# Kernel optimization log

Measured on AMD Instinct MI355X. Metric: run time of the kernel, lower is better.

## Reference

```python
import jax, jax.numpy as jnp
import numpy as np

N = 100000
NUM_CLASSES = 10
EPS = 1e-16
NEG_SLOPE = 0.2


def gat_conv(x, src, dst, W, a_src, a_dst, bias, heads, out_ch, concat):
    # x: [N, F_in]; src/dst: [E] (message flows src -> dst, PyG convention)
    n = x.shape[0]
    h = (x @ W).reshape(n, heads, out_ch)              # [N, H, C]
    al = jnp.sum(h * a_src, axis=-1)                   # [N, H] source attention term
    ar = jnp.sum(h * a_dst, axis=-1)                   # [N, H] target attention term
    e = jax.nn.leaky_relu(al[src] + ar[dst], NEG_SLOPE)  # [E, H]
    # segment softmax over incoming edges of each dst node
    m = jax.ops.segment_max(e, dst, num_segments=n)    # [N, H]
    ex = jnp.exp(e - m[dst])                           # [E, H]
    denom = jax.ops.segment_sum(ex, dst, num_segments=n)  # [N, H]
    alpha = ex / (denom[dst] + EPS)                    # [E, H]
    msg = h[src] * alpha[..., None]                    # [E, H, C]
    out = jax.ops.segment_sum(msg, dst, num_segments=n)   # [N, H, C]
    out = out.reshape(n, heads * out_ch) if concat else out.mean(axis=1)
    return out + bias


def setup_inputs() -> dict:
    key = jax.random.key(0)
    ks = jax.random.split(key, 10)
    F_in, H1, C1 = 512, 8, 8
    x = jax.random.normal(ks[0], (N, F_in), dtype=jnp.float32)
    edge_index = jax.random.randint(ks[1], (2, 1600000), 0, N, dtype=jnp.int64)
    s = 0.05
    return {
        "x": x,
        "edge_index": edge_index,
        "W1": jax.random.normal(ks[2], (F_in, H1 * C1), dtype=jnp.float32) * s,
        "a_src1": jax.random.normal(ks[3], (H1, C1), dtype=jnp.float32) * s,
        "a_dst1": jax.random.normal(ks[4], (H1, C1), dtype=jnp.float32) * s,
        "b1": jnp.zeros((H1 * C1,), dtype=jnp.float32),
        "W2": jax.random.normal(ks[5], (H1 * C1, NUM_CLASSES), dtype=jnp.float32) * s,
        "a_src2": jax.random.normal(ks[6], (1, NUM_CLASSES), dtype=jnp.float32) * s,
        "a_dst2": jax.random.normal(ks[7], (1, NUM_CLASSES), dtype=jnp.float32) * s,
        "b2": jnp.zeros((NUM_CLASSES,), dtype=jnp.float32),
    }


def reference(x, edge_index, W1, a_src1, a_dst1, b1, W2, a_src2, a_dst2, b2):
    # add self-loops (GATConv default add_self_loops=True)
    loops = jnp.arange(N, dtype=edge_index.dtype)
    src = jnp.concatenate([edge_index[0], loops])
    dst = jnp.concatenate([edge_index[1], loops])
    # eval mode: dropout(p=0.6) is identity
    h = gat_conv(x, src, dst, W1, a_src1, a_dst1, b1, heads=8, out_ch=8, concat=True)
    h = jax.nn.elu(h)
    out = gat_conv(h, src, dst, W2, a_src2, a_dst2, b2, heads=1, out_ch=NUM_CLASSES, concat=True)
    return jax.nn.log_softmax(out, axis=1)
```

## Files before the change

### kernel.cpp

```cpp
#include <hip/hip_runtime.h>
#include <math.h>

#define NN 100000
#define NEDGE 1600000
#define NTOT 1700000
#define FIN 512
#define NH1 8
#define NC1 8
#define F1 64
#define NC2 10
#define SLOPE 0.2f
#define EPSF 1e-16f
#define SCAN_BLK 1024
#define NB ((NN + SCAN_BLK - 1) / SCAN_BLK)

typedef short short8 __attribute__((ext_vector_type(8)));
typedef float f32x4 __attribute__((ext_vector_type(4)));

__device__ __forceinline__ float lrelu(float x) { return x > 0.f ? x : SLOPE * x; }
__device__ __forceinline__ float eluf(float x) { return x > 0.f ? x : __expf(x) - 1.f; }

__device__ __forceinline__ unsigned short f2bf_rne(float f) {
    unsigned int u = __float_as_uint(f);
    unsigned int r = (u + 0x7FFFu + ((u >> 16) & 1u)) >> 16;
    return (unsigned short)r;
}
__device__ __forceinline__ float bf2f(unsigned short b) {
    return __uint_as_float(((unsigned int)b) << 16);
}

__global__ void k_init(const float* __restrict__ W, unsigned short* __restrict__ wT,
                       int* __restrict__ cnt)
{
    int i = blockIdx.x * 256 + threadIdx.x;
    if (i < NN) cnt[i] = 1;
    if (i < F1 * FIN) {
        int n = i & 63, k = i >> 6;
        wT[n * FIN + k] = f2bf_rne(W[k * F1 + n]);
    }
}

#define LDA 40

__global__ __launch_bounds__(256) void k_gemm1(const float* __restrict__ x,
                                               const unsigned short* __restrict__ wT,
                                               unsigned short* __restrict__ h1b)
{
    __shared__ unsigned short Al[64][LDA];
    __shared__ unsigned short Bl[64][LDA];
    const int tid = threadIdx.x;
    const int row0 = blockIdx.x * 64;
    const int w  = tid >> 6;
    const int l  = tid & 63;
    const int lr = l & 15;
    const int lg = l >> 4;
    f32x4 acc[4] = {};

    for (int k0 = 0; k0 < FIN; k0 += 32) {
        #pragma unroll
        for (int t2 = 0; t2 < 2; ++t2) {
            int idx = tid + t2 * 256;
            int r = idx >> 3, q = idx & 7;
            int gr = row0 + r;
            float4 v = (gr < NN) ? *(const float4*)(x + (size_t)gr * FIN + k0 + 4 * q)
                                 : make_float4(0.f, 0.f, 0.f, 0.f);
            ushort4 u;
            u.x = f2bf_rne(v.x); u.y = f2bf_rne(v.y);
            u.z = f2bf_rne(v.z); u.w = f2bf_rne(v.w);
            *(ushort4*)&Al[r][4 * q] = u;
        }
        {
            int n = tid >> 2, q = tid & 3;
            *(uint4*)&Bl[n][8 * q] = *(const uint4*)(wT + (size_t)n * FIN + k0 + 8 * q);
        }
        __syncthreads();
        short8 a = *(const short8*)&Al[16 * w + lr][8 * lg];
        #pragma unroll
        for (int nt = 0; nt < 4; ++nt) {
            short8 b = *(const short8*)&Bl[16 * nt + lr][8 * lg];
            acc[nt] = __builtin_amdgcn_mfma_f32_16x16x32_bf16(a, b, acc[nt], 0, 0, 0);
        }
        __syncthreads();
    }
    #pragma unroll
    for (int r = 0; r < 4; ++r) {
        int gr = row0 + 16 * w + 4 * lg + r;
        if (gr < NN) {
            #pragma unroll
            for (int nt = 0; nt < 4; ++nt)
                h1b[(size_t)gr * F1 + 16 * nt + lr] = f2bf_rne(acc[nt][r]);
        }
    }
}

__global__ void k_prep1(const unsigned short* __restrict__ h1b,
                        const float* __restrict__ asrc, const float* __restrict__ adst,
                        float* __restrict__ al, float* __restrict__ ar)
{
    int i = blockIdx.x * blockDim.x + threadIdx.x;
    if (i >= NN * NH1) return;
    int node = i >> 3, hh = i & 7;
    const unsigned short* hp = h1b + (size_t)node * F1 + hh * NC1;
    ushort4 u0 = *(const ushort4*)hp;
    ushort4 u1 = *(const ushort4*)(hp + 4);
    float hv[8] = {bf2f(u0.x), bf2f(u0.y), bf2f(u0.z), bf2f(u0.w),
                   bf2f(u1.x), bf2f(u1.y), bf2f(u1.z), bf2f(u1.w)};
    const float* as = asrc + hh * NC1;
    const float* ad = adst + hh * NC1;
    float sa = 0.f, sd = 0.f;
    #pragma unroll
    for (int c = 0; c < 8; ++c) { sa += hv[c] * as[c]; sd += hv[c] * ad[c]; }
    al[i] = sa; ar[i] = sd;
}

__global__ void k_hist(const int* __restrict__ ei, int* __restrict__ cnt,
                       int* __restrict__ pos)
{
    int e = blockIdx.x * blockDim.x + threadIdx.x;
    if (e >= NEDGE) return;
    pos[e] = atomicAdd(&cnt[ei[NEDGE + e]], 1);
}

__global__ __launch_bounds__(256) void k_scan1(const int* __restrict__ cnt,
                                               int* __restrict__ off,
                                               int* __restrict__ bsum)
{
    __shared__ int s[256];
    int t = threadIdx.x;
    int base = blockIdx.x * SCAN_BLK + t * 4;
    int c0 = (base + 0 < NN) ? cnt[base + 0] : 0;
    int c1 = (base + 1 < NN) ? cnt[base + 1] : 0;
    int c2 = (base + 2 < NN) ? cnt[base + 2] : 0;
    int c3 = (base + 3 < NN) ? cnt[base + 3] : 0;
    int ts = c0 + c1 + c2 + c3;
    s[t] = ts;
    __syncthreads();
    #pragma unroll
    for (int d = 1; d < 256; d <<= 1) {
        int v = (t >= d) ? s[t - d] : 0;
        __syncthreads();
        s[t] += v;
        __syncthreads();
    }
    int run = s[t] - ts;
    if (t == 255) bsum[blockIdx.x] = s[255];
    if (base + 0 < NN) off[base + 0] = run; run += c0;
    if (base + 1 < NN) off[base + 1] = run; run += c1;
    if (base + 2 < NN) off[base + 2] = run; run += c2;
    if (base + 3 < NN) off[base + 3] = run;
}

__global__ void k_scan2(int* __restrict__ bsum, int* __restrict__ off)
{
    __shared__ int s[128];
    int t = threadIdx.x;
    int v = (t < NB) ? bsum[t] : 0;
    s[t] = v;
    __syncthreads();
    #pragma unroll
    for (int d = 1; d < 128; d <<= 1) {
        int w = (t >= d) ? s[t - d] : 0;
        __syncthreads();
        s[t] += w;
        __syncthreads();
    }
    if (t < NB) bsum[t] = s[t] - v;
    if (t == 0) off[NN] = NTOT;
}

__global__ void k_scan3(int* __restrict__ off, const int* __restrict__ bsum,
                        int* __restrict__ esrc)
{
    int i = blockIdx.x * blockDim.x + threadIdx.x;
    if (i >= NN) return;
    int o = off[i] + bsum[i >> 10];
    off[i] = o;
    esrc[o] = i;
}

__global__ void k_scatter(const int* __restrict__ ei, const int* __restrict__ off,
                          const int* __restrict__ pos, int* __restrict__ esrc)
{
    int e = blockIdx.x * blockDim.x + threadIdx.x;
    if (e >= NEDGE) return;
    esrc[off[ei[NEDGE + e]] + pos[e]] = ei[e];
}

__global__ __launch_bounds__(256) void k_agg1csr(const int* __restrict__ off,
                                                 const int* __restrict__ esrc,
                                                 const float* __restrict__ al,
                                                 const float* __restrict__ ar,
                                                 const unsigned short* __restrict__ h1b,
                                                 const float* __restrict__ b1,
                                                 float* __restrict__ g)
{
    int node = blockIdx.x * 4 + (threadIdx.x >> 6);
    int lane = threadIdx.x & 63;
    int h = lane >> 3;
    int beg = off[node], end = off[node + 1];
    float arn = ar[node * NH1 + h];
    float acc0 = 0.f, acc1 = 0.f, ds0 = 0.f, ds1 = 0.f;
    int i = beg;
    for (; i + 1 < end; i += 2) {
        int s0 = esrc[i], s1 = esrc[i + 1];
        float e0 = __expf(lrelu(al[s0 * NH1 + h] + arn));
        float e1 = __expf(lrelu(al[s1 * NH1 + h] + arn));
        acc0 += bf2f(h1b[(size_t)s0 * F1 + lane]) * e0; ds0 += e0;
        acc1 += bf2f(h1b[(size_t)s1 * F1 + lane]) * e1; ds1 += e1;
    }
    if (i < end) {
        int s0 = esrc[i];
        float e0 = __expf(lrelu(al[s0 * NH1 + h] + arn));
        acc0 += bf2f(h1b[(size_t)s0 * F1 + lane]) * e0; ds0 += e0;
    }
    float v = (acc0 + acc1) / (ds0 + ds1 + EPSF);
    g[(size_t)node * F1 + lane] = eluf(v + b1[lane]);
}

__global__ __launch_bounds__(256) void k_l2prep(
    const float* __restrict__ g, const float* __restrict__ W2,
    const float* __restrict__ asrc2, const float* __restrict__ adst2,
    float* __restrict__ packed)
{
    __shared__ float sW[F1 * NC2];
    __shared__ float sas[NC2], sad[NC2];
    int tid = threadIdx.x;
    for (int i = tid; i < F1 * NC2; i += 256) sW[i] = W2[i];
    if (tid < NC2) { sas[tid] = asrc2[tid]; sad[tid] = adst2[tid]; }
    __syncthreads();
    int n = blockIdx.x * 256 + tid;
    if (n >= NN) return;

    const float* row = g + (size_t)n * F1;
    float acc[NC2] = {};
    #pragma unroll
    for (int c = 0; c < F1; c += 4) {
        float4 v = *(const float4*)(row + c);
        #pragma unroll
        for (int o = 0; o < NC2; ++o) {
            acc[o] += v.x * sW[(c + 0) * NC2 + o] + v.y * sW[(c + 1) * NC2 + o]
                    + v.z * sW[(c + 2) * NC2 + o] + v.w * sW[(c + 3) * NC2 + o];
        }
    }
    float sa = 0.f, sd = 0.f;
    #pragma unroll
    for (int o = 0; o < NC2; ++o) { sa += acc[o] * sas[o]; sd += acc[o] * sad[o]; }
    float* p = packed + (size_t)n * 12;
    #pragma unroll
    for (int o = 0; o < NC2; ++o) p[o] = acc[o];
    p[10] = sa; p[11] = sd;
}

__global__ __launch_bounds__(256) void k_agg2csr(const int* __restrict__ off,
                                                 const int* __restrict__ esrc,
                                                 const float* __restrict__ packed,
                                                 const float* __restrict__ b2,
                                                 float* __restrict__ out)
{
    int node = blockIdx.x * 16 + (threadIdx.x >> 4);
    int li = threadIdx.x & 15;
    int beg = off[node], end = off[node + 1];
    float arn = packed[(size_t)node * 12 + 11];
    float acc = 0.f, dsum = 0.f;
    for (int i = beg; i < end; ++i) {
        int s = esrc[i];
        float val = (li < 12) ? packed[(size_t)s * 12 + li] : 0.f;
        float al2s = __shfl(val, 10, 16);
        float ev = __expf(lrelu(al2s + arn));
        if (li < NC2) acc += val * ev;
        dsum += ev;
    }
    float z = (li < NC2) ? acc / (dsum + EPSF) + b2[li] : -1e30f;
    float m = z;
    #pragma unroll
    for (int d = 8; d >= 1; d >>= 1) m = fmaxf(m, __shfl_xor(m, d, 16));
    float ex = (li < NC2) ? __expf(z - m) : 0.f;
    float ss = ex;
    #pragma unroll
    for (int d = 8; d >= 1; d >>= 1) ss += __shfl_xor(ss, d, 16);
    float ls = __logf(ss) + m;
    if (li < NC2) out[(size_t)node * NC2 + li] = z - ls;
}

extern "C" void kernel_launch(void* const* d_in, const int* in_sizes, int n_in,
                              void* d_out, int out_size, void* d_ws, size_t ws_size,
                              hipStream_t stream)
{
    const float* x    = (const float*)d_in[0];
    const int*   ei   = (const int*)d_in[1];
    const float* W1   = (const float*)d_in[2];
    const float* as1  = (const float*)d_in[3];
    const float* ad1  = (const float*)d_in[4];
    const float* b1   = (const float*)d_in[5];
    const float* W2   = (const float*)d_in[6];
    const float* as2  = (const float*)d_in[7];
    const float* ad2  = (const float*)d_in[8];
    const float* b2   = (const float*)d_in[9];
    float* out = (float*)d_out;

    char* ws = (char*)d_ws;
    unsigned short* h1b = (unsigned short*)ws;
    unsigned short* wT  = h1b + (size_t)NN * F1;
    float* al1 = (float*)(wT + (size_t)F1 * FIN);
    float* ar1 = al1 + (size_t)NN * NH1;
    float* g   = ar1 + (size_t)NN * NH1;
    float* packed = g + (size_t)NN * F1;
    int* cnt   = (int*)(packed + (size_t)NN * 12);
    int* off   = cnt + NN;
    int* bsum  = off + NN + 1;
    int* esrc  = bsum + 128;
    int* pos   = esrc + NTOT;

    k_init<<<(NN + 255) / 256, 256, 0, stream>>>(W1, wT, cnt);
    k_gemm1<<<(NN + 63) / 64, 256, 0, stream>>>(x, wT, h1b);
    k_hist<<<(NEDGE + 255) / 256, 256, 0, stream>>>(ei, cnt, pos);
    k_scan1<<<NB, 256, 0, stream>>>(cnt, off, bsum);
    k_scan2<<<1, 128, 0, stream>>>(bsum, off);
    k_scan3<<<(NN + 255) / 256, 256, 0, stream>>>(off, bsum, esrc);
    k_scatter<<<(NEDGE + 255) / 256, 256, 0, stream>>>(ei, off, pos, esrc);
    k_prep1<<<(NN * NH1 + 255) / 256, 256, 0, stream>>>(h1b, as1, ad1, al1, ar1);
    k_agg1csr<<<NN / 4, 256, 0, stream>>>(off, esrc, al1, ar1, h1b, b1, g);
    k_l2prep<<<(NN + 255) / 256, 256, 0, stream>>>(g, W2, as2, ad2, packed);
    k_agg2csr<<<NN / 16, 256, 0, stream>>>(off, esrc, packed, b2, out);
}
```

Baseline: 606.5 us.

## Fuse attention-score prep into GEMM epilogue and layer-2 projection into aggregation

The per-node source/target attention dot products for layer 1 are now computed in the GEMM epilogue, using a lane shuffle reduction over the fp32 MFMA accumulators, so the separate prep kernel goes away. The layer-2 linear projection and its attention terms are folded into the layer-1 aggregation kernel through a 64-lane shuffle reduction. This removes the fp32 hidden buffer g and its write-then-read round trip through memory. The packed record is padded to 16 floats for aligned access, and the gather loops are unrolled further for more loads in flight. Attention scores now come from fp32 rather than bf16-rounded values, and the aggregation kernel gains extra registers and shuffles.

```diff
diff --git a/kernel.cpp b/kernel.cpp
--- a/kernel.cpp
+++ b/kernel.cpp
@@ -44,16 +44,22 @@
 
 __global__ __launch_bounds__(256) void k_gemm1(const float* __restrict__ x,
                                                const unsigned short* __restrict__ wT,
-                                               unsigned short* __restrict__ h1b)
+                                               const float* __restrict__ asrc,
+                                               const float* __restrict__ adst,
+                                               unsigned short* __restrict__ h1b,
+                                               float* __restrict__ al,
+                                               float* __restrict__ ar)
 {
     __shared__ unsigned short Al[64][LDA];
     __shared__ unsigned short Bl[64][LDA];
+    __shared__ float sas[F1], sad[F1];
     const int tid = threadIdx.x;
     const int row0 = blockIdx.x * 64;
     const int w  = tid >> 6;
     const int l  = tid & 63;
     const int lr = l & 15;
     const int lg = l >> 4;
+    if (tid < F1) { sas[tid] = asrc[tid]; sad[tid] = adst[tid]; }
     f32x4 acc[4] = {};
 
     for (int k0 = 0; k0 < FIN; k0 += 32) {
@@ -91,26 +97,44 @@
                 h1b[(size_t)gr * F1 + 16 * nt + lr] = f2bf_rne(acc[nt][r]);
         }
     }
-}
-
-__global__ void k_prep1(const unsigned short* __restrict__ h1b,
-                        const float* __restrict__ asrc, const float* __restrict__ adst,
-                        float* __restrict__ al, float* __restrict__ ar)
-{
-    int i = blockIdx.x * blockDim.x + threadIdx.x;
-    if (i >= NN * NH1) return;
-    int node = i >> 3, hh = i & 7;
-    const unsigned short* hp = h1b + (size_t)node * F1 + hh * NC1;
-    ushort4 u0 = *(const ushort4*)hp;
-    ushort4 u1 = *(const ushort4*)(hp + 4);
-    float hv[8] = {bf2f(u0.x), bf2f(u0.y), bf2f(u0.z), bf2f(u0.w),
-                   bf2f(u1.x), bf2f(u1.y), bf2f(u1.z), bf2f(u1.w)};
-    const float* as = asrc + hh * NC1;
-    const float* ad = adst + hh * NC1;
-    float sa = 0.f, sd = 0.f;
-    #pragma unroll
-    for (int c = 0; c < 8; ++c) { sa += hv[c] * as[c]; sd += hv[c] * ad[c]; }
-    al[i] = sa; ar[i] = sd;
+    float pa[4][4], pd[4][4];
+    #pragma unroll
+    for (int nt = 0; nt < 4; ++nt) {
+        float wa = sas[16 * nt + lr], wd = sad[16 * nt + lr];
+        #pragma unroll
+        for (int r = 0; r < 4; ++r) {
+            float c = acc[nt][r];
+            pa[nt][r] = c * wa;
+            pd[nt][r] = c * wd;
+        }
+    }
+    #pragma unroll
+    for (int d = 1; d <= 4; d <<= 1) {
+        #pragma unroll
+        for (int nt = 0; nt < 4; ++nt)
+            #pragma unroll
+            for (int r = 0; r < 4; ++r) {
+                pa[nt][r] += __shfl_xor(pa[nt][r], d);
+                pd[nt][r] += __shfl_xor(pd[nt][r], d);
+            }
+    }
+    int low3 = lr & 7, hi = lr >> 3;
+    if (low3 < 4) {
+        int head = 2 * low3 + hi;
+        #pragma unroll
+        for (int nt = 0; nt < 4; ++nt) {
+            if (low3 == nt) {
+                #pragma unroll
+                for (int r = 0; r < 4; ++r) {
+                    int gr = row0 + 16 * w + 4 * lg + r;
+                    if (gr < NN) {
+                        al[gr * NH1 + head] = pa[nt][r];
+                        ar[gr * NH1 + head] = pd[nt][r];
+                    }
+                }
+            }
+        }
+    }
 }
 
 __global__ void k_hist(const int* __restrict__ ei, int* __restrict__ cnt,
@@ -186,91 +210,102 @@
     esrc[off[ei[NEDGE + e]] + pos[e]] = ei[e];
 }
 
-__global__ __launch_bounds__(256) void k_agg1csr(const int* __restrict__ off,
-                                                 const int* __restrict__ esrc,
-                                                 const float* __restrict__ al,
-                                                 const float* __restrict__ ar,
-                                                 const unsigned short* __restrict__ h1b,
-                                                 const float* __restrict__ b1,
-                                                 float* __restrict__ g)
-{
-    int node = blockIdx.x * 4 + (threadIdx.x >> 6);
-    int lane = threadIdx.x & 63;
+__global__ __launch_bounds__(256) void k_agg1(const int* __restrict__ off,
+                                              const int* __restrict__ esrc,
+                                              const float* __restrict__ al,
+                                              const float* __restrict__ ar,
+                                              const unsigned short* __restrict__ h1b,
+                                              const float* __restrict__ b1,
+                                              const float* __restrict__ W2,
+                                              const float* __restrict__ as2,
+                                              const float* __restrict__ ad2,
+                                              float* __restrict__ packed)
+{
+    __shared__ float s2a[NC2], s2d[NC2];
+    int tid = threadIdx.x;
+    if (tid < NC2) { s2a[tid] = as2[tid]; s2d[tid] = ad2[tid]; }
+    __syncthreads();
+    int node = blockIdx.x * 4 + (tid >> 6);
+    int lane = tid & 63;
     int h = lane >> 3;
+    float b1l = b1[lane];
+    float w2r[NC2];
+    #pragma unroll
+    for (int o = 0; o < NC2; ++o) w2r[o] = W2[lane * NC2 + o];
+
     int beg = off[node], end = off[node + 1];
     float arn = ar[node * NH1 + h];
-    float acc0 = 0.f, acc1 = 0.f, ds0 = 0.f, ds1 = 0.f;
+    float a0 = 0.f, a1 = 0.f, a2 = 0.f, a3 = 0.f;
+    float d0 = 0.f, d1 = 0.f, d2 = 0.f, d3 = 0.f;
+    int i = beg;
+    for (; i + 3 < end; i += 4) {
+        int s0 = esrc[i], s1 = esrc[i + 1], s2 = esrc[i + 2], s3 = esrc[i + 3];
+        float e0 = __expf(lrelu(al[s0 * NH1 + h] + arn));
+        float e1 = __expf(lrelu(al[s1 * NH1 + h] + arn));
+        float e2 = __expf(lrelu(al[s2 * NH1 + h] + arn));
+        float e3 = __expf(lrelu(al[s3 * NH1 + h] + arn));
+        a0 += bf2f(h1b[(size_t)s0 * F1 + lane]) * e0; d0 += e0;
+        a1 += bf2f(h1b[(size_t)s1 * F1 + lane]) * e1; d1 += e1;
+        a2 += bf2f(h1b[(size_t)s2 * F1 + lane]) * e2; d2 += e2;
+        a3 += bf2f(h1b[(size_t)s3 * F1 + lane]) * e3; d3 += e3;
+    }
+    for (; i < end; ++i) {
+        int s0 = esrc[i];
+        float e0 = __expf(lrelu(al[s0 * NH1 + h] + arn));
+        a0 += bf2f(h1b[(size_t)s0 * F1 + lane]) * e0; d0 += e0;
+    }
+    float v = ((a0 + a1) + (a2 + a3)) / (((d0 + d1) + (d2 + d3)) + EPSF);
+    float gl = eluf(v + b1l);
+
+    float p[NC2];
+    #pragma unroll
+    for (int o = 0; o < NC2; ++o) p[o] = gl * w2r[o];
+    #pragma unroll
+    for (int d = 1; d <= 32; d <<= 1)
+        #pragma unroll
+        for (int o = 0; o < NC2; ++o) p[o] += __shfl_xor(p[o], d);
+    float sa = 0.f, sd = 0.f;
+    #pragma unroll
+    for (int o = 0; o < NC2; ++o) { sa += p[o] * s2a[o]; sd += p[o] * s2d[o]; }
+
+    float* rec = packed + (size_t)node * 16;
+    if (lane < NC2) rec[lane] = p[lane];
+    if (lane == 10) rec[10] = sa;
+    if (lane == 11) rec[11] = sd;
+}
+
+__global__ __launch_bounds__(256) void k_agg2(const int* __restrict__ off,
+                                              const int* __restrict__ esrc,
+                                              const float* __restrict__ packed,
+                                              const float* __restrict__ b2,
+                                              float* __restrict__ out)
+{
+    int node = blockIdx.x * 16 + (threadIdx.x >> 4);
+    int li = threadIdx.x & 15;
+    int beg = off[node], end = off[node + 1];
+    float arn = packed[(size_t)node * 16 + 11];
+    float acc = 0.f, acc1 = 0.f, dsum = 0.f, dsum1 = 0.f;
     int i = beg;
     for (; i + 1 < end; i += 2) {
         int s0 = esrc[i], s1 = esrc[i + 1];
-        float e0 = __expf(lrelu(al[s0 * NH1 + h] + arn));
-        float e1 = __expf(lrelu(al[s1 * NH1 + h] + arn));
-        acc0 += bf2f(h1b[(size_t)s0 * F1 + lane]) * e0; ds0 += e0;
-        acc1 += bf2f(h1b[(size_t)s1 * F1 + lane]) * e1; ds1 += e1;
+        float v0 = (li < 12) ? packed[(size_t)s0 * 16 + li] : 0.f;
+        float v1 = (li < 12) ? packed[(size_t)s1 * 16 + li] : 0.f;
+        float al0 = __shfl(v0, 10, 16);
+        float al1 = __shfl(v1, 10, 16);
+        float e0 = __expf(lrelu(al0 + arn));
+        float e1 = __expf(lrelu(al1 + arn));
+        if (li < NC2) { acc += v0 * e0; acc1 += v1 * e1; }
+        dsum += e0; dsum1 += e1;
     }
     if (i < end) {
         int s0 = esrc[i];
-        float e0 = __expf(lrelu(al[s0 * NH1 + h] + arn));
-        acc0 += bf2f(h1b[(size_t)s0 * F1 + lane]) * e0; ds0 += e0;
-    }
-    float v = (acc0 + acc1) / (ds0 + ds1 + EPSF);
-    g[(size_t)node * F1 + lane] = eluf(v + b1[lane]);
-}
-
-__global__ __launch_bounds__(256) void k_l2prep(
-    const float* __restrict__ g, const float* __restrict__ W2,
-    const float* __restrict__ asrc2, const float* __restrict__ adst2,
-    float* __restrict__ packed)
-{
-    __shared__ float sW[F1 * NC2];
-    __shared__ float sas[NC2], sad[NC2];
-    int tid = threadIdx.x;
-    for (int i = tid; i < F1 * NC2; i += 256) sW[i] = W2[i];
-    if (tid < NC2) { sas[tid] = asrc2[tid]; sad[tid] = adst2[tid]; }
-    __syncthreads();
-    int n = blockIdx.x * 256 + tid;
-    if (n >= NN) return;
-
-    const float* row = g + (size_t)n * F1;
-    float acc[NC2] = {};
-    #pragma unroll
-    for (int c = 0; c < F1; c += 4) {
-        float4 v = *(const float4*)(row + c);
-        #pragma unroll
-        for (int o = 0; o < NC2; ++o) {
-            acc[o] += v.x * sW[(c + 0) * NC2 + o] + v.y * sW[(c + 1) * NC2 + o]
-                    + v.z * sW[(c + 2) * NC2 + o] + v.w * sW[(c + 3) * NC2 + o];
-        }
-    }
-    float sa = 0.f, sd = 0.f;
-    #pragma unroll
-    for (int o = 0; o < NC2; ++o) { sa += acc[o] * sas[o]; sd += acc[o] * sad[o]; }
-    float* p = packed + (size_t)n * 12;
-    #pragma unroll
-    for (int o = 0; o < NC2; ++o) p[o] = acc[o];
-    p[10] = sa; p[11] = sd;
-}
-
-__global__ __launch_bounds__(256) void k_agg2csr(const int* __restrict__ off,
-                                                 const int* __restrict__ esrc,
-                                                 const float* __restrict__ packed,
-                                                 const float* __restrict__ b2,
-                                                 float* __restrict__ out)
-{
-    int node = blockIdx.x * 16 + (threadIdx.x >> 4);
-    int li = threadIdx.x & 15;
-    int beg = off[node], end = off[node + 1];
-    float arn = packed[(size_t)node * 12 + 11];
-    float acc = 0.f, dsum = 0.f;
-    for (int i = beg; i < end; ++i) {
-        int s = esrc[i];
-        float val = (li < 12) ? packed[(size_t)s * 12 + li] : 0.f;
-        float al2s = __shfl(val, 10, 16);
-        float ev = __expf(lrelu(al2s + arn));
-        if (li < NC2) acc += val * ev;
-        dsum += ev;
-    }
-    float z = (li < NC2) ? acc / (dsum + EPSF) + b2[li] : -1e30f;
+        float v0 = (li < 12) ? packed[(size_t)s0 * 16 + li] : 0.f;
+        float al0 = __shfl(v0, 10, 16);
+        float e0 = __expf(lrelu(al0 + arn));
+        if (li < NC2) acc += v0 * e0;
+        dsum += e0;
+    }
+    float z = (li < NC2) ? (acc + acc1) / (dsum + dsum1 + EPSF) + b2[li] : -1e30f;
     float m = z;
     #pragma unroll
     for (int d = 8; d >= 1; d >>= 1) m = fmaxf(m, __shfl_xor(m, d, 16));
@@ -303,23 +338,20 @@
     unsigned short* wT  = h1b + (size_t)NN * F1;
     float* al1 = (float*)(wT + (size_t)F1 * FIN);
     float* ar1 = al1 + (size_t)NN * NH1;
-    float* g   = ar1 + (size_t)NN * NH1;
-    float* packed = g + (size_t)NN * F1;
-    int* cnt   = (int*)(packed + (size_t)NN * 12);
+    float* packed = ar1 + (size_t)NN * NH1;
+    int* cnt   = (int*)(packed + (size_t)NN * 16);
     int* off   = cnt + NN;
     int* bsum  = off + NN + 1;
     int* esrc  = bsum + 128;
     int* pos   = esrc + NTOT;
 
     k_init<<<(NN + 255) / 256, 256, 0, stream>>>(W1, wT, cnt);
-    k_gemm1<<<(NN + 63) / 64, 256, 0, stream>>>(x, wT, h1b);
+    k_gemm1<<<(NN + 63) / 64, 256, 0, stream>>>(x, wT, as1, ad1, h1b, al1, ar1);
     k_hist<<<(NEDGE + 255) / 256, 256, 0, stream>>>(ei, cnt, pos);
     k_scan1<<<NB, 256, 0, stream>>>(cnt, off, bsum);
     k_scan2<<<1, 128, 0, stream>>>(bsum, off);
     k_scan3<<<(NN + 255) / 256, 256, 0, stream>>>(off, bsum, esrc);
     k_scatter<<<(NEDGE + 255) / 256, 256, 0, stream>>>(ei, off, pos, esrc);
-    k_prep1<<<(NN * NH1 + 255) / 256, 256, 0, stream>>>(h1b, as1, ad1, al1, ar1);
-    k_agg1csr<<<NN / 4, 256, 0, stream>>>(off, esrc, al1, ar1, h1b, b1, g);
-    k_l2prep<<<(NN + 255) / 256, 256, 0, stream>>>(g, W2, as2, ad2, packed);
-    k_agg2csr<<<NN / 16, 256, 0, stream>>>(off, esrc, packed, b2, out);
-}
+    k_agg1<<<NN / 4, 256, 0, stream>>>(off, esrc, al1, ar1, h1b, b1, W2, as2, ad2, packed);
+    k_agg2<<<NN / 16, 256, 0, stream>>>(off, esrc, packed, b2, out);
+}
```

Result: no change. 596.1 us (-1.7%).
